# Performance work log

Measured on AMD Instinct MI355X. Metric: run time of the kernel, lower is better.

## Reference

```python
import jax, jax.numpy as jnp
import numpy as np

M = 12288   # anchor nodes
N = 12288   # neighbor nodes
D = 128     # out_features
TEMPERATURE = 0.07
NEG_PAD = jnp.float32(-2**32 + 1)  # same padding constant as torch code


def setup_inputs() -> dict:
    key = jax.random.key(0)
    k1, k2, k3, k4 = jax.random.split(key, 4)
    xx_anchor = jax.random.normal(k1, (M, D), dtype=jnp.float32)
    inp = jax.random.normal(k2, (N, D), dtype=jnp.float32)
    # sparse binary adjacency (~avg degree 25), stored dense int32 since the
    # module calls adj.to_dense() and only tests adj > 0
    adj = (jax.random.uniform(k3, (M, N)) < 0.002).astype(jnp.int32)
    # xavier_uniform-style init for the [D, D] attention weight
    limit = jnp.sqrt(6.0 / (D + D)).astype(jnp.float32)
    weight = jax.random.uniform(k4, (D, D), minval=-limit, maxval=limit, dtype=jnp.float32)
    return {"xx_anchor": xx_anchor, "input": inp, "adj": adj, "weight": weight}


def reference(xx_anchor, input, adj, weight):
    # scores[m, n] = (xx_anchor @ W) . input_n   -> dense [M, N]
    anchor_adj = jnp.einsum('md,de,ne->mn', xx_anchor, weight, input)
    scores = jnp.where(adj > 0, anchor_adj, NEG_PAD)
    atten = jax.nn.softmax(scores / TEMPERATURE, axis=1)  # row softmax over neighbors
    return atten @ input  # [M, D]
```

## Files before the change

### kernel.cpp

```cpp
#include <hip/hip_runtime.h>
#include <hip/hip_bf16.h>

#define M_ROWS 12288
#define N_COLS 12288
#define DDIM   128
#define MAXD   256
#define INV_T  (1.0f / 0.07f)

typedef int v4i __attribute__((ext_vector_type(4)));

__global__ __launch_bounds__(256, 4)
void layerconv_fused(const float* __restrict__ xa,
                     const float* __restrict__ inp,
                     const int*   __restrict__ adj,
                     const float* __restrict__ wgt,
                     float*       __restrict__ out)
{
    __shared__ int idx[4][MAXD];
    __shared__ int scnt[4];

    const int lane = threadIdx.x & 63;
    const int wid  = threadIdx.x >> 6;
    const int m    = blockIdx.x * 4 + wid;

    if (lane == 0) scnt[wid] = 0;

    const float2 xv = ((const float2*)(xa + (size_t)m * DDIM))[lane];
    float y0 = 0.f, y1 = 0.f;
    {
        const float2* wrow = (const float2*)wgt;
        #pragma unroll 8
        for (int k = 0; k < DDIM; ++k) {
            const float  xak = __shfl((k & 1) ? xv.y : xv.x, k >> 1);
            const float2 w   = wrow[(size_t)k * 64 + lane];
            y0 = fmaf(xak, w.x, y0);
            y1 = fmaf(xak, w.y, y1);
        }
    }

    {
        const v4i* arow = (const v4i*)(adj + (size_t)m * N_COLS);
        #pragma unroll 4
        for (int i = lane; i < N_COLS / 4; i += 64) {
            const v4i a = __builtin_nontemporal_load(&arow[i]);
            if ((a.x | a.y | a.z | a.w) != 0) {
                const int k = (a.x > 0) + (a.y > 0) + (a.z > 0) + (a.w > 0);
                int p = atomicAdd(&scnt[wid], k);
                if (p + k <= MAXD) {
                    if (a.x > 0) idx[wid][p++] = 4*i + 0;
                    if (a.y > 0) idx[wid][p++] = 4*i + 1;
                    if (a.z > 0) idx[wid][p++] = 4*i + 2;
                    if (a.w > 0) idx[wid][p  ] = 4*i + 3;
                }
            }
        }
    }
    const int cn = min(scnt[wid], MAXD);

    float mrun = -INFINITY, lrun = 0.f, a0 = 0.f, a1 = 0.f;
    for (int j = 0; j < cn; ++j) {
        const int    n = idx[wid][j];
        const float2 v = ((const float2*)(inp + (size_t)n * DDIM))[lane];
        float s = fmaf(y0, v.x, y1 * v.y);
        #pragma unroll
        for (int off = 1; off < 64; off <<= 1) s += __shfl_xor(s, off);
        s *= INV_T;
        const float mnew  = fmaxf(mrun, s);
        const float scale = __expf(mrun - mnew);
        const float e     = __expf(s - mnew);
        lrun = fmaf(lrun, scale, e);
        a0   = fmaf(a0, scale, e * v.x);
        a1   = fmaf(a1, scale, e * v.y);
        mrun = mnew;
    }

    if (cn > 0) {
        const float inv = 1.f / lrun;
        a0 *= inv; a1 *= inv;
    } else {
        for (int n = 0; n < N_COLS; ++n) {
            const float2 v = ((const float2*)(inp + (size_t)n * DDIM))[lane];
            a0 += v.x; a1 += v.y;
        }
        a0 *= (1.f / N_COLS); a1 *= (1.f / N_COLS);
    }
    ((float2*)(out + (size_t)m * DDIM))[lane] = make_float2(a0, a1);
}

extern "C" void kernel_launch(void* const* d_in, const int* in_sizes, int n_in,
                              void* d_out, int out_size, void* d_ws, size_t ws_size,
                              hipStream_t stream) {
    const float* xa  = (const float*)d_in[0];
    const float* inp = (const float*)d_in[1];
    const int*   adj = (const int*)d_in[2];
    const float* wgt = (const float*)d_in[3];
    float* out = (float*)d_out;

    layerconv_fused<<<M_ROWS / 4, 256, 0, stream>>>(xa, inp, adj, wgt, out);
}
```

Measured before the change: 817.4 us.

## Assign one row per block and split scan and softmax across waves

Each block now processes a single anchor row. All 256 threads scan the adjacency row cooperatively into a shared index list, and the four waves split the neighbour gather with an online softmax each. The per-wave partial max, sum and accumulators are then merged in shared memory. This shortens the serial per-row latency chain and raises the occupancy hint. The cost is redundant x·W computation in every wave and extra block-level synchronisation.

After: 900.8 us. +10.2%, slower.

```diff
diff --git a/kernel.cpp b/kernel.cpp
--- a/kernel.cpp
+++ b/kernel.cpp
@@ -1,5 +1,4 @@
 #include <hip/hip_runtime.h>
-#include <hip/hip_bf16.h>
 
 #define M_ROWS 12288
 #define N_COLS 12288
@@ -9,21 +8,43 @@
 
 typedef int v4i __attribute__((ext_vector_type(4)));
 
-__global__ __launch_bounds__(256, 4)
+__global__ __launch_bounds__(256, 8)
 void layerconv_fused(const float* __restrict__ xa,
                      const float* __restrict__ inp,
                      const int*   __restrict__ adj,
                      const float* __restrict__ wgt,
                      float*       __restrict__ out)
 {
-    __shared__ int idx[4][MAXD];
-    __shared__ int scnt[4];
+    __shared__ int    idx[MAXD];
+    __shared__ int    scnt;
+    __shared__ float  red_m[4];
+    __shared__ float  red_l[4];
+    __shared__ float2 red_a[4][64];
 
     const int lane = threadIdx.x & 63;
     const int wid  = threadIdx.x >> 6;
-    const int m    = blockIdx.x * 4 + wid;
+    const int m    = blockIdx.x;
 
-    if (lane == 0) scnt[wid] = 0;
+    if (threadIdx.x == 0) scnt = 0;
+    __syncthreads();
+
+    {
+        const v4i* arow = (const v4i*)(adj + (size_t)m * N_COLS);
+        #pragma unroll 4
+        for (int i = threadIdx.x; i < N_COLS / 4; i += 256) {
+            const v4i a = __builtin_nontemporal_load(&arow[i]);
+            if ((a.x | a.y | a.z | a.w) != 0) {
+                const int k = (a.x > 0) + (a.y > 0) + (a.z > 0) + (a.w > 0);
+                int p = atomicAdd(&scnt, k);
+                if (p + k <= MAXD) {
+                    if (a.x > 0) idx[p++] = 4*i + 0;
+                    if (a.y > 0) idx[p++] = 4*i + 1;
+                    if (a.z > 0) idx[p++] = 4*i + 2;
+                    if (a.w > 0) idx[p  ] = 4*i + 3;
+                }
+            }
+        }
+    }
 
     const float2 xv = ((const float2*)(xa + (size_t)m * DDIM))[lane];
     float y0 = 0.f, y1 = 0.f;
@@ -38,28 +59,12 @@
         }
     }
 
-    {
-        const v4i* arow = (const v4i*)(adj + (size_t)m * N_COLS);
-        #pragma unroll 4
-        for (int i = lane; i < N_COLS / 4; i += 64) {
-            const v4i a = __builtin_nontemporal_load(&arow[i]);
-            if ((a.x | a.y | a.z | a.w) != 0) {
-                const int k = (a.x > 0) + (a.y > 0) + (a.z > 0) + (a.w > 0);
-                int p = atomicAdd(&scnt[wid], k);
-                if (p + k <= MAXD) {
-                    if (a.x > 0) idx[wid][p++] = 4*i + 0;
-                    if (a.y > 0) idx[wid][p++] = 4*i + 1;
-                    if (a.z > 0) idx[wid][p++] = 4*i + 2;
-                    if (a.w > 0) idx[wid][p  ] = 4*i + 3;
-                }
-            }
-        }
-    }
-    const int cn = min(scnt[wid], MAXD);
+    __syncthreads();
+    const int cn = min(scnt, MAXD);
 
     float mrun = -INFINITY, lrun = 0.f, a0 = 0.f, a1 = 0.f;
-    for (int j = 0; j < cn; ++j) {
-        const int    n = idx[wid][j];
+    for (int j = wid; j < cn; j += 4) {
+        const int    n = idx[j];
         const float2 v = ((const float2*)(inp + (size_t)n * DDIM))[lane];
         float s = fmaf(y0, v.x, y1 * v.y);
         #pragma unroll
@@ -74,17 +79,35 @@
         mrun = mnew;
     }
 
-    if (cn > 0) {
-        const float inv = 1.f / lrun;
-        a0 *= inv; a1 *= inv;
-    } else {
-        for (int n = 0; n < N_COLS; ++n) {
-            const float2 v = ((const float2*)(inp + (size_t)n * DDIM))[lane];
-            a0 += v.x; a1 += v.y;
+    if (lane == 0) { red_m[wid] = mrun; red_l[wid] = lrun; }
+    red_a[wid][lane] = make_float2(a0, a1);
+    __syncthreads();
+
+    if (wid == 0) {
+        if (cn > 0) {
+            const float mstar = fmaxf(fmaxf(red_m[0], red_m[1]),
+                                      fmaxf(red_m[2], red_m[3]));
+            float l = 0.f, b0 = 0.f, b1 = 0.f;
+            #pragma unroll
+            for (int w = 0; w < 4; ++w) {
+                const float  sc = __expf(red_m[w] - mstar);
+                const float2 aw = red_a[w][lane];
+                l  = fmaf(red_l[w], sc, l);
+                b0 = fmaf(aw.x, sc, b0);
+                b1 = fmaf(aw.y, sc, b1);
+            }
+            const float inv = 1.f / l;
+            ((float2*)(out + (size_t)m * DDIM))[lane] = make_float2(b0 * inv, b1 * inv);
+        } else {
+            float b0 = 0.f, b1 = 0.f;
+            for (int n = 0; n < N_COLS; ++n) {
+                const float2 v = ((const float2*)(inp + (size_t)n * DDIM))[lane];
+                b0 += v.x; b1 += v.y;
+            }
+            ((float2*)(out + (size_t)m * DDIM))[lane] =
+                make_float2(b0 * (1.f / N_COLS), b1 * (1.f / N_COLS));
         }
-        a0 *= (1.f / N_COLS); a1 *= (1.f / N_COLS);
     }
-    ((float2*)(out + (size_t)m * DDIM))[lane] = make_float2(a0, a1);
 }
 
 extern "C" void kernel_launch(void* const* d_in, const int* in_sizes, int n_in,
@@ -96,5 +119,5 @@
     const float* wgt = (const float*)d_in[3];
     float* out = (float*)d_out;
 
-    layerconv_fused<<<M_ROWS / 4, 256, 0, stream>>>(xa, inp, adj, wgt, out);
+    layerconv_fused<<<M_ROWS, 256, 0, stream>>>(xa, inp, adj, wgt, out);
 }
```
